# Kernel tuning notes

Hardware: AMD Instinct MI355X
Metric: run time of the kernel (lower is better)

## Reference

```python
import jax, jax.numpy as jnp
import numpy as np

N_NODES = 40000
N_EDGES = 320000
IN_DIM = 256
HID = 128
HEADS = 4
N_GAT = 3  # num_layers - 1
EPS = 1e-5
NEG_SLOPE = 0.2  # PyG GATConv default


def setup_inputs() -> dict:
    key = jax.random.key(0)
    ks = jax.random.split(key, 16)
    s = 0.05
    return {
        "x": jax.random.normal(ks[0], (N_NODES, IN_DIM), jnp.float32),
        "edge_index": jax.random.randint(ks[1], (2, N_EDGES), 0, N_NODES, jnp.int64),
        "proj_W": jax.random.normal(ks[2], (IN_DIM, HID), jnp.float32) * s,
        "proj_b": jnp.zeros((HID,), jnp.float32),
        "gat_W": jax.random.normal(ks[3], (N_GAT, HID, HEADS * HID), jnp.float32) * s,
        "gat_att_src": jax.random.normal(ks[4], (N_GAT, HEADS, HID), jnp.float32) * s,
        "gat_att_dst": jax.random.normal(ks[5], (N_GAT, HEADS, HID), jnp.float32) * s,
        "gat_bias": jnp.zeros((N_GAT, HID), jnp.float32),
        "ln_gamma": jnp.ones((N_GAT, HID), jnp.float32),
        "ln_beta": jnp.zeros((N_GAT, HID), jnp.float32),
        "gcn_W": jax.random.normal(ks[6], (HID, 1), jnp.float32) * s,
        "gcn_b": jnp.zeros((1,), jnp.float32),
    }


def reference(x, edge_index, proj_W, proj_b, gat_W, gat_att_src, gat_att_dst,
              gat_bias, ln_gamma, ln_beta, gcn_W, gcn_b):
    N = x.shape[0]
    loops = jnp.arange(N)
    src = jnp.concatenate([edge_index[0], loops])  # add_self_loops=True
    dst = jnp.concatenate([edge_index[1], loops])

    h = x @ proj_W + proj_b  # [N, HID]

    for i in range(N_GAT):
        identity = h
        xh = (h @ gat_W[i]).reshape(N, HEADS, HID)      # [N, H, C]
        a_s = jnp.einsum("nhc,hc->nh", xh, gat_att_src[i])  # [N, H]
        a_d = jnp.einsum("nhc,hc->nh", xh, gat_att_dst[i])
        e = jax.nn.leaky_relu(a_s[src] + a_d[dst], NEG_SLOPE)  # [E, H]
        # segment softmax over incoming edges per dst node
        m = jax.ops.segment_max(e, dst, num_segments=N)
        ex = jnp.exp(e - m[dst])
        denom = jax.ops.segment_sum(ex, dst, num_segments=N)
        alpha = ex / denom[dst]                         # [E, H]
        agg = jax.ops.segment_sum(xh[src] * alpha[:, :, None], dst, num_segments=N)
        h = agg.mean(axis=1) + gat_bias[i]              # concat=False -> head mean
        # LayerNorm (biased variance, eps=1e-5)
        mu = h.mean(-1, keepdims=True)
        var = ((h - mu) ** 2).mean(-1, keepdims=True)
        h = (h - mu) * jax.lax.rsqrt(var + EPS) * ln_gamma[i] + ln_beta[i]
        h = jax.nn.relu(h)
        # dropout: inference mode -> identity
        h = h + identity

    # GCNConv(hidden, 1) with symmetric normalization and self loops
    deg = jax.ops.segment_sum(jnp.ones_like(dst, dtype=h.dtype), dst, num_segments=N)
    dinv = jax.lax.rsqrt(deg)  # deg >= 1 due to self loops
    norm = dinv[src] * dinv[dst]                        # [E]
    xw = h @ gcn_W                                      # [N, 1]
    out = jax.ops.segment_sum(xw[src] * norm[:, None], dst, num_segments=N) + gcn_b
    return jax.nn.sigmoid(out).reshape(-1)
```

## Files before the change

kernel.cpp:

```cpp
#include <hip/hip_runtime.h>
#include <math.h>

#define INDIM 256
#define HID 128
#define HEADS 4
#define NGAT 3
#define LN_EPS 1e-5f
#define SLOPE 0.2f
#define MPAD 40064
#define LOG2E 1.4426950408889634f

typedef __attribute__((ext_vector_type(8))) short short8;
typedef __attribute__((ext_vector_type(4))) float f32x4;

__device__ inline float wsum(float v) {
#pragma unroll
  for (int m = 1; m < 64; m <<= 1) v += __shfl_xor(v, m, 64);
  return v;
}
__device__ inline float wmax(float v) {
#pragma unroll
  for (int m = 1; m < 64; m <<= 1) v = fmaxf(v, __shfl_xor(v, m, 64));
  return v;
}
__device__ inline float lk2(float v) { return fmaxf(v, SLOPE * v) * LOG2E; }
__device__ inline float sel4(float a0, float a1, float a2, float a3, int i) {
  float lo = (i & 1) ? a1 : a0;
  float hi = (i & 1) ? a3 : a2;
  return (i & 2) ? hi : lo;
}

__device__ inline unsigned short f2b(float f) {
  unsigned u = __float_as_uint(f);
  unsigned r = (u + 0x7FFFu + ((u >> 16) & 1u)) >> 16;
  return (unsigned short)r;
}
__device__ inline float b2f(unsigned short b) {
  return __uint_as_float(((unsigned)b) << 16);
}
__device__ inline void unp8(const uint4 v, float f[8]) {
  f[0] = __uint_as_float(v.x << 16);
  f[1] = __uint_as_float(v.x & 0xFFFF0000u);
  f[2] = __uint_as_float(v.y << 16);
  f[3] = __uint_as_float(v.y & 0xFFFF0000u);
  f[4] = __uint_as_float(v.z << 16);
  f[5] = __uint_as_float(v.z & 0xFFFF0000u);
  f[6] = __uint_as_float(v.w << 16);
  f[7] = __uint_as_float(v.w & 0xFFFF0000u);
}

__device__ __host__ inline size_t fidx(int row, int k, int K) {
  return ((size_t)(row >> 4) * (K >> 5) + (k >> 5)) * 512 +
         ((((k >> 3) & 3) * 16 + (row & 15)) << 3) + (k & 7);
}

__global__ void k_deg(const int* __restrict__ ei, int E, int N, int* __restrict__ deg) {
  int e = blockIdx.x * blockDim.x + threadIdx.x;
  if (e >= E + N) return;
  int dst = (e < E) ? ei[E + e] : (e - E);
  atomicAdd(&deg[dst], 1);
}

__global__ void k_scan1(const int* __restrict__ deg, int N, int* __restrict__ bsums) {
  __shared__ int s[256];
  int gid = blockIdx.x * 256 + threadIdx.x;
  s[threadIdx.x] = (gid < N) ? deg[gid] : 0;
  __syncthreads();
  for (int off = 128; off > 0; off >>= 1) {
    if (threadIdx.x < off) s[threadIdx.x] += s[threadIdx.x + off];
    __syncthreads();
  }
  if (threadIdx.x == 0) bsums[blockIdx.x] = s[0];
}

__global__ void k_scan2(int* __restrict__ bsums, int nblk, int* __restrict__ rowptr, int N) {
  __shared__ int s[256];
  int t = threadIdx.x;
  int v = (t < nblk) ? bsums[t] : 0;
  s[t] = v;
  __syncthreads();
  for (int off = 1; off < 256; off <<= 1) {
    int u = (t >= off) ? s[t - off] : 0;
    __syncthreads();
    s[t] += u;
    __syncthreads();
  }
  if (t < nblk) bsums[t] = s[t] - v;
  if (t == nblk - 1) rowptr[N] = s[t];
}

__global__ void k_scan3(const int* __restrict__ deg, int N, const int* __restrict__ bsums,
                        int* __restrict__ rowptr, int* __restrict__ cursor,
                        float* __restrict__ dinv) {
  __shared__ int s[256];
  int gid = blockIdx.x * 256 + threadIdx.x;
  int v = (gid < N) ? deg[gid] : 0;
  s[threadIdx.x] = v;
  __syncthreads();
  for (int off = 1; off < 256; off <<= 1) {
    int t = (threadIdx.x >= off) ? s[threadIdx.x - off] : 0;
    __syncthreads();
    s[threadIdx.x] += t;
    __syncthreads();
  }
  if (gid < N) {
    int ex = bsums[blockIdx.x] + s[threadIdx.x] - v;
    rowptr[gid] = ex;
    cursor[gid] = ex;
    dinv[gid] = rsqrtf((float)v);
  }
}

__global__ void k_fill(const int* __restrict__ ei, int E, int N,
                       int* __restrict__ cursor, int* __restrict__ csr) {
  int e = blockIdx.x * blockDim.x + threadIdx.x;
  if (e >= E + N) return;
  int src, dst;
  if (e < E) { src = ei[e]; dst = ei[E + e]; } else { src = dst = e - E; }
  int pos = atomicAdd(&cursor[dst], 1);
  csr[pos] = src;
}

__global__ void k_wprep(const float* __restrict__ Wp, const float* __restrict__ Wg,
                        unsigned short* __restrict__ WtPF,
                        unsigned short* __restrict__ Wt2F) {
  int idx = blockIdx.x * 256 + threadIdx.x;
  if (idx < INDIM * HID) {
    int k = idx >> 7, c = idx & 127;
    WtPF[fidx(c, k, INDIM)] = f2b(Wp[idx]);
    return;
  }
  idx -= INDIM * HID;
  if (idx >= NGAT * HID * HEADS * HID) return;
  int l = idx / (HID * HEADS * HID);
  int rem = idx - l * HID * HEADS * HID;
  int k = rem >> 9;
  int cc = rem & 511;
  int hh = cc >> 7, c = cc & 127;
  Wt2F[(size_t)l * (HID * HEADS * HID) + fidx(c, hh * HID + k, HEADS * HID)] =
      f2b(Wg[idx] * 0.25f);
}

__global__ void k_xfrag(const float* __restrict__ x, unsigned short* __restrict__ xbF,
                        int N) {
  int t = blockIdx.x * 256 + threadIdx.x;
  if (t >= MPAD * 32) return;
  int n = t >> 5, kc = t & 31;
  uint4 pk = make_uint4(0, 0, 0, 0);
  if (n < N) {
    const float* ap = x + (size_t)n * INDIM + kc * 8;
    float4 u = *(const float4*)ap;
    float4 v = *(const float4*)(ap + 4);
    pk.x = (unsigned)f2b(u.x) | ((unsigned)f2b(u.y) << 16);
    pk.y = (unsigned)f2b(u.z) | ((unsigned)f2b(u.w) << 16);
    pk.z = (unsigned)f2b(v.x) | ((unsigned)f2b(v.y) << 16);
    pk.w = (unsigned)f2b(v.z) | ((unsigned)f2b(v.w) << 16);
  }
  size_t addr = ((size_t)(n >> 4) * 8 + (kc >> 2)) * 512 +
                (((kc & 3) * 16 + (n & 15)) << 3);
  *(uint4*)(xbF + addr) = pk;
}

__global__ void k_wvec(const float* __restrict__ W, const float* __restrict__ atts,
                       const float* __restrict__ attd, float* __restrict__ w_s,
                       float* __restrict__ w_d) {
  int lane = threadIdx.x & 63;
  int idx = blockIdx.x * 4 + (threadIdx.x >> 6);
  if (idx >= NGAT * HEADS * HID) return;
  int l = idx / (HEADS * HID);
  int rem = idx - l * (HEADS * HID);
  int hh = rem >> 7, k = rem & 127;
  const float2 w2 = *(const float2*)(W + ((size_t)(l * HID + k)) * (HEADS * HID) +
                                     hh * HID + lane * 2);
  const float2 s2 = *(const float2*)(atts + (size_t)(l * HEADS + hh) * HID + lane * 2);
  const float2 d2 = *(const float2*)(attd + (size_t)(l * HEADS + hh) * HID + lane * 2);
  float ps = w2.x * s2.x + w2.y * s2.y;
  float pd = w2.x * d2.x + w2.y * d2.y;
  ps = wsum(ps);
  pd = wsum(pd);
  if (lane == 0) { w_s[idx] = ps; w_d[idx] = pd; }
}

__global__ __launch_bounds__(256) void k_mm(
    const unsigned short* __restrict__ xbF, const unsigned short* __restrict__ WtPF,
    const float* __restrict__ bias, const float* __restrict__ ws0,
    const float* __restrict__ wd0, unsigned short* __restrict__ hb,
    float* __restrict__ a_s, float* __restrict__ a_d) {
  const int wid = threadIdx.x >> 6;
  const int lane = threadIdx.x & 63;
  const int l15 = lane & 15;
  const int g = lane >> 4;
  const int row0 = blockIdx.x * 64 + wid * 16;
  f32x4 acc[8] = {};
  const unsigned short* Ap = xbF + (size_t)(row0 >> 4) * 8 * 512 + lane * 8;
  const unsigned short* Bp = WtPF + lane * 8;
  for (int kb = 0; kb < 8; ++kb) {
    short8 af = *(const short8*)(Ap + kb * 512);
    short8 bfr[8];
#pragma unroll
    for (int ni = 0; ni < 8; ++ni)
      bfr[ni] = *(const short8*)(Bp + (size_t)(ni * 8 + kb) * 512);
#pragma unroll
    for (int ni = 0; ni < 8; ++ni)
      acc[ni] = __builtin_amdgcn_mfma_f32_16x16x32_bf16(af, bfr[ni], acc[ni], 0, 0, 0);
  }
#pragma unroll
  for (int r = 0; r < 4; ++r) {
    const int row = row0 + g * 4 + r;
    unsigned short* hbr = hb + (size_t)row * HID;
    float yv[8];
#pragma unroll
    for (int ni = 0; ni < 8; ++ni) {
      const int c = ni * 16 + l15;
      yv[ni] = acc[ni][r] + bias[c];
      hbr[c] = f2b(yv[ni]);
    }
    float ps[4], pd[4];
#pragma unroll
    for (int h4 = 0; h4 < 4; ++h4) {
      float pv = 0.f, qv = 0.f;
#pragma unroll
      for (int ni = 0; ni < 8; ++ni) {
        const int c = h4 * HID + ni * 16 + l15;
        pv = fmaf(yv[ni], ws0[c], pv);
        qv = fmaf(yv[ni], wd0[c], qv);
      }
#pragma unroll
      for (int m = 1; m < 16; m <<= 1) {
        pv += __shfl_xor(pv, m, 64);
        qv += __shfl_xor(qv, m, 64);
      }
      ps[h4] = pv;
      pd[h4] = qv;
    }
    if (l15 == 0) {
      *(float4*)(a_s + (size_t)row * 4) = make_float4(ps[0], ps[1], ps[2], ps[3]);
      *(float4*)(a_d + (size_t)row * 4) = make_float4(pd[0], pd[1], pd[2], pd[3]);
    }
  }
}

__global__ __launch_bounds__(256) void k_agg2(
    const int* __restrict__ rowptr, const int* __restrict__ csr,
    const unsigned short* __restrict__ hb, const float* __restrict__ a_s,
    const float* __restrict__ a_d, unsigned short* __restrict__ aggF, int N) {
  __shared__ int s_lds[4][64];
  __shared__ float al_lds[4][4][68];
  int lane = threadIdx.x & 63;
  int wid = threadIdx.x >> 6;
  int n = blockIdx.x * 4 + wid;
  if (n >= MPAD) return;
  const int g = lane >> 4;
  const int l15 = lane & 15;
  size_t oaddr = ((size_t)(n >> 4) * 16 + (g * 4 + (l15 >> 2))) * 512 +
                 (((l15 & 3) * 16 + (n & 15)) << 3);
  if (n >= N) {
    *(uint4*)(aggF + oaddr) = make_uint4(0, 0, 0, 0);
    return;
  }
  int beg = rowptr[n], end = rowptr[n + 1];
  int deg = end - beg;
  const unsigned short* hbase = hb + l15 * 8;
  float acc[8] = {};
  float f[8];
  if (deg <= 64) {
    const float ad = a_d[n * 4 + g];
    int sj[4];
    float ex[4];
    float mymax = -3e38f;
#pragma unroll
    for (int j = 0; j < 4; ++j) {
      int e = beg + l15 + 16 * j;
      bool v = e < end;
      int s = v ? csr[e] : 0;
      sj[j] = s;
      float Lv = v ? lk2(a_s[s * 4 + g] + ad) : -3e38f;
      ex[j] = Lv;
      mymax = fmaxf(mymax, Lv);
    }
#pragma unroll
    for (int m = 1; m < 16; m <<= 1) mymax = fmaxf(mymax, __shfl_xor(mymax, m, 64));
    float mysum = 0.f;
#pragma unroll
    for (int j = 0; j < 4; ++j) {
      ex[j] = exp2f(ex[j] - mymax);
      mysum += ex[j];
    }
#pragma unroll
    for (int m = 1; m < 16; m <<= 1) mysum += __shfl_xor(mysum, m, 64);
    float r = 1.f / mysum;
#pragma unroll
    for (int j = 0; j < 4; ++j) {
      int i = l15 + 16 * j;
      al_lds[wid][g][i] = ex[j] * r;
      if (g == 0) s_lds[wid][i] = sj[j];
    }
    asm volatile("s_waitcnt lgkmcnt(0)" ::: "memory");
    const int* sw = s_lds[wid];
    const float* aw = al_lds[wid][g];
    int nIter = (deg + 3) >> 2;
    for (int it = 0; it < nIter; ++it) {
      int4 s4 = *(const int4*)(sw + it * 4);
      float4 a4 = *(const float4*)(aw + it * 4);
      uint4 r0 = *(const uint4*)(hbase + (size_t)s4.x * HID);
      uint4 r1 = *(const uint4*)(hbase + (size_t)s4.y * HID);
      uint4 r2 = *(const uint4*)(hbase + (size_t)s4.z * HID);
      uint4 r3 = *(const uint4*)(hbase + (size_t)s4.w * HID);
      unp8(r0, f);
#pragma unroll
      for (int j = 0; j < 8; ++j) acc[j] = fmaf(a4.x, f[j], acc[j]);
      unp8(r1, f);
#pragma unroll
      for (int j = 0; j < 8; ++j) acc[j] = fmaf(a4.y, f[j], acc[j]);
      unp8(r2, f);
#pragma unroll
      for (int j = 0; j < 8; ++j) acc[j] = fmaf(a4.z, f[j], acc[j]);
      unp8(r3, f);
#pragma unroll
      for (int j = 0; j < 8; ++j) acc[j] = fmaf(a4.w, f[j], acc[j]);
    }
  } else {
    const float4 adv = *(const float4*)(a_d + (size_t)n * 4);
    float m0 = -3e38f, m1 = -3e38f, m2 = -3e38f, m3 = -3e38f;
    for (int e = beg + lane; e < end; e += 64) {
      int s = csr[e];
      const float4 asv = *(const float4*)(a_s + (size_t)s * 4);
      m0 = fmaxf(m0, lk2(asv.x + adv.x));
      m1 = fmaxf(m1, lk2(asv.y + adv.y));
      m2 = fmaxf(m2, lk2(asv.z + adv.z));
      m3 = fmaxf(m3, lk2(asv.w + adv.w));
    }
    m0 = wmax(m0); m1 = wmax(m1); m2 = wmax(m2); m3 = wmax(m3);
    float d0 = 0.f, d1 = 0.f, d2 = 0.f, d3 = 0.f;
    for (int e = beg + lane; e < end; e += 64) {
      int s = csr[e];
      const float4 asv = *(const float4*)(a_s + (size_t)s * 4);
      d0 += exp2f(lk2(asv.x + adv.x) - m0);
      d1 += exp2f(lk2(asv.y + adv.y) - m1);
      d2 += exp2f(lk2(asv.z + adv.z) - m2);
      d3 += exp2f(lk2(asv.w + adv.w) - m3);
    }
    float r0 = 1.f / wsum(d0);
    float r1 = 1.f / wsum(d1);
    float r2 = 1.f / wsum(d2);
    float r3 = 1.f / wsum(d3);
    for (int sb = beg; sb < end; sb += 64) {
      int e = sb + lane;
      bool val = e < end;
      int s = csr[val ? e : end - 1];
      const float4 asv = *(const float4*)(a_s + (size_t)s * 4);
      float q0 = val ? exp2f(lk2(asv.x + adv.x) - m0) * r0 : 0.f;
      float q1 = val ? exp2f(lk2(asv.y + adv.y) - m1) * r1 : 0.f;
      float q2 = val ? exp2f(lk2(asv.z + adv.z) - m2) * r2 : 0.f;
      float q3 = val ? exp2f(lk2(asv.w + adv.w) - m3) * r3 : 0.f;
      int cnt = min(64, end - sb);
      for (int i = 0; i < cnt; ++i) {
        int si = __shfl(s, i, 64);
        float c0 = __shfl(q0, i, 64), c1 = __shfl(q1, i, 64);
        float c2 = __shfl(q2, i, 64), c3 = __shfl(q3, i, 64);
        uint4 hv = *(const uint4*)(hbase + (size_t)si * HID);
        float bi = sel4(c0, c1, c2, c3, g);
        unp8(hv, f);
#pragma unroll
        for (int j = 0; j < 8; ++j) acc[j] = fmaf(bi, f[j], acc[j]);
      }
    }
  }
  uint4 pk;
  pk.x = (unsigned)f2b(acc[0]) | ((unsigned)f2b(acc[1]) << 16);
  pk.y = (unsigned)f2b(acc[2]) | ((unsigned)f2b(acc[3]) << 16);
  pk.z = (unsigned)f2b(acc[4]) | ((unsigned)f2b(acc[5]) << 16);
  pk.w = (unsigned)f2b(acc[6]) | ((unsigned)f2b(acc[7]) << 16);
  *(uint4*)(aggF + oaddr) = pk;
}

template <int ATT>
__global__ __launch_bounds__(256) void k_mm2(
    const unsigned short* __restrict__ aggF, const unsigned short* __restrict__ Bt,
    const float* __restrict__ bias, const float* __restrict__ gamma,
    const float* __restrict__ beta, const float* __restrict__ wsn,
    const float* __restrict__ wdn, unsigned short* __restrict__ hb,
    float* __restrict__ a_s, float* __restrict__ a_d, float* __restrict__ xw) {
  const int wid = threadIdx.x >> 6;
  const int lane = threadIdx.x & 63;
  const int l15 = lane & 15;
  const int g = lane >> 4;
  const int row0 = blockIdx.x * 64 + wid * 16;
  f32x4 acc[8] = {};
  const unsigned short* Ap = aggF + (size_t)(row0 >> 4) * 16 * 512 + lane * 8;
  const unsigned short* Bp = Bt + lane * 8;
  for (int kb = 0; kb < 16; ++kb) {
    short8 a0 = *(const short8*)(Ap + kb * 512);
    short8 bfr[8];
#pragma unroll
    for (int ni = 0; ni < 8; ++ni)
      bfr[ni] = *(const short8*)(Bp + (size_t)(ni * 16 + kb) * 512);
#pragma unroll
    for (int ni = 0; ni < 8; ++ni)
      acc[ni] = __builtin_amdgcn_mfma_f32_16x16x32_bf16(a0, bfr[ni], acc[ni], 0, 0, 0);
  }
  float gm[8], bt8[8];
#pragma unroll
  for (int ni = 0; ni < 8; ++ni) {
    int c = ni * 16 + l15;
    gm[ni] = gamma[c];
    bt8[ni] = beta[c];
    float bs = bias[c];
#pragma unroll
    for (int r = 0; r < 4; ++r) acc[ni][r] += bs;
  }
#pragma unroll
  for (int r = 0; r < 4; ++r) {
    float s = 0.f;
#pragma unroll
    for (int ni = 0; ni < 8; ++ni) s += acc[ni][r];
#pragma unroll
    for (int m = 1; m < 16; m <<= 1) s += __shfl_xor(s, m, 64);
    float mu = s * (1.f / 128.f);
    float q = 0.f;
#pragma unroll
    for (int ni = 0; ni < 8; ++ni) {
      float dd = acc[ni][r] - mu;
      q += dd * dd;
    }
#pragma unroll
    for (int m = 1; m < 16; m <<= 1) q += __shfl_xor(q, m, 64);
    float rstd = rsqrtf(q * (1.f / 128.f) + LN_EPS);
    const int row = row0 + g * 4 + r;
    unsigned short* hbr = hb + (size_t)row * HID;
    float yv[8];
#pragma unroll
    for (int ni = 0; ni < 8; ++ni) {
      int c = ni * 16 + l15;
      float y = (acc[ni][r] - mu) * rstd * gm[ni] + bt8[ni];
      y = fmaxf(y, 0.f) + b2f(hbr[c]);
      hbr[c] = f2b(y);
      yv[ni] = y;
    }
    if (ATT == 1) {
      float ps[4], pd[4];
#pragma unroll
      for (int h4 = 0; h4 < 4; ++h4) {
        float pv = 0.f, qv = 0.f;
#pragma unroll
        for (int ni = 0; ni < 8; ++ni) {
          const int c = h4 * HID + ni * 16 + l15;
          pv = fmaf(yv[ni], wsn[c], pv);
          qv = fmaf(yv[ni], wdn[c], qv);
        }
#pragma unroll
        for (int m = 1; m < 16; m <<= 1) {
          pv += __shfl_xor(pv, m, 64);
          qv += __shfl_xor(qv, m, 64);
        }
        ps[h4] = pv;
        pd[h4] = qv;
      }
      if (l15 == 0) {
        *(float4*)(a_s + (size_t)row * 4) = make_float4(ps[0], ps[1], ps[2], ps[3]);
        *(float4*)(a_d + (size_t)row * 4) = make_float4(pd[0], pd[1], pd[2], pd[3]);
      }
    } else {
      float pv = 0.f;
#pragma unroll
      for (int ni = 0; ni < 8; ++ni) pv = fmaf(yv[ni], wsn[ni * 16 + l15], pv);
#pragma unroll
      for (int m = 1; m < 16; m <<= 1) pv += __shfl_xor(pv, m, 64);
      if (l15 == 0) xw[row] = pv;
    }
  }
}

__global__ __launch_bounds__(256) void k_gcn(const int* __restrict__ rowptr,
                                             const int* __restrict__ csr,
                                             const float* __restrict__ xw,
                                             const float* __restrict__ dinv,
                                             const float* __restrict__ gcn_b,
                                             float* __restrict__ out, int N) {
  int n = blockIdx.x * blockDim.x + threadIdx.x;
  if (n >= N) return;
  float acc = 0.f;
  int beg = rowptr[n], end = rowptr[n + 1];
  for (int e = beg; e < end; ++e) {
    int s = csr[e];
    acc += xw[s] * dinv[s];
  }
  float z = acc * dinv[n] + gcn_b[0];
  out[n] = 1.f / (1.f + expf(-z));
}

extern "C" void kernel_launch(void* const* d_in, const int* in_sizes, int n_in,
                              void* d_out, int out_size, void* d_ws, size_t ws_size,
                              hipStream_t stream) {
  const float* x = (const float*)d_in[0];
  const int* ei = (const int*)d_in[1];
  const float* proj_W = (const float*)d_in[2];
  const float* proj_b = (const float*)d_in[3];
  const float* gat_W = (const float*)d_in[4];
  const float* gat_as = (const float*)d_in[5];
  const float* gat_ad = (const float*)d_in[6];
  const float* gat_bias = (const float*)d_in[7];
  const float* ln_g = (const float*)d_in[8];
  const float* ln_b = (const float*)d_in[9];
  const float* gcn_W = (const float*)d_in[10];
  const float* gcn_b = (const float*)d_in[11];
  float* out = (float*)d_out;

  const int N = in_sizes[0] / INDIM;
  const int E = in_sizes[1] / 2;
  const int TOT = E + N;

  size_t off = 0;
  auto alloc = [&](size_t bytes) {
    void* p = (char*)d_ws + off;
    off += (bytes + 255) & ~(size_t)255;
    return p;
  };
  unsigned short* hb = (unsigned short*)alloc((size_t)MPAD * HID * 2);
  unsigned short* aggF = (unsigned short*)alloc((size_t)MPAD * HEADS * HID * 2);
  unsigned short* xbF = (unsigned short*)alloc((size_t)MPAD * INDIM * 2);
  unsigned short* WtPF = (unsigned short*)alloc((size_t)HID * INDIM * 2);
  unsigned short* Wt2F = (unsigned short*)alloc((size_t)NGAT * HID * HEADS * HID * 2);
  float* w_s = (float*)alloc((size_t)NGAT * HEADS * HID * 4);
  float* w_d = (float*)alloc((size_t)NGAT * HEADS * HID * 4);
  float* a_s = (float*)alloc((size_t)MPAD * HEADS * 4);
  float* a_d = (float*)alloc((size_t)MPAD * HEADS * 4);
  int* deg = (int*)alloc((size_t)N * 4);
  int* rowptr = (int*)alloc((size_t)(N + 1) * 4);
  int* cursor = (int*)alloc((size_t)N * 4);
  int* csr = (int*)alloc((size_t)TOT * 4);
  int* bsums = (int*)alloc(1024);
  float* dinv = (float*)alloc((size_t)N * 4);
  float* xw = (float*)alloc((size_t)MPAD * 4);
  (void)ws_size;

  const int NBLK = (N + 255) / 256;
  const int EBLK = (TOT + 255) / 256;

  hipMemsetAsync(deg, 0, (size_t)N * 4, stream);
  k_deg<<<EBLK, 256, 0, stream>>>(ei, E, N, deg);
  k_scan1<<<NBLK, 256, 0, stream>>>(deg, N, bsums);
  k_scan2<<<1, 256, 0, stream>>>(bsums, NBLK, rowptr, N);
  k_scan3<<<NBLK, 256, 0, stream>>>(deg, N, bsums, rowptr, cursor, dinv);
  k_fill<<<EBLK, 256, 0, stream>>>(ei, E, N, cursor, csr);

  const int WPN = INDIM * HID + NGAT * HID * HEADS * HID;
  k_wprep<<<(WPN + 255) / 256, 256, 0, stream>>>(proj_W, gat_W, WtPF, Wt2F);
  k_wvec<<<(NGAT * HEADS * HID + 3) / 4, 256, 0, stream>>>(gat_W, gat_as, gat_ad, w_s, w_d);
  k_xfrag<<<(MPAD * 32 + 255) / 256, 256, 0, stream>>>(x, xbF, N);

  k_mm<<<MPAD / 64, 256, 0, stream>>>(xbF, WtPF, proj_b, w_s, w_d, hb, a_s, a_d);

  for (int i = 0; i < NGAT; ++i) {
    k_agg2<<<MPAD / 4, 256, 0, stream>>>(rowptr, csr, hb, a_s, a_d, aggF, N);
    if (i < NGAT - 1) {
      k_mm2<1><<<MPAD / 64, 256, 0, stream>>>(
          aggF, Wt2F + (size_t)i * HID * HEADS * HID, gat_bias + (size_t)i * HID,
          ln_g + (size_t)i * HID, ln_b + (size_t)i * HID,
          w_s + (size_t)(i + 1) * HEADS * HID, w_d + (size_t)(i + 1) * HEADS * HID,
          hb, a_s, a_d, nullptr);
    } else {
      k_mm2<2><<<MPAD / 64, 256, 0, stream>>>(
          aggF, Wt2F + (size_t)i * HID * HEADS * HID, gat_bias + (size_t)i * HID,
          ln_g + (size_t)i * HID, ln_b + (size_t)i * HID, gcn_W, nullptr,
          hb, nullptr, nullptr, xw);
    }
  }

  k_gcn<<<NBLK, 256, 0, stream>>>(rowptr, csr, xw, dinv, gcn_b, out, N);
}
```

Before: 280.3 us.

## Fuse x bf16 conversion into projection GEMM and prescale GCN features

```diff
diff --git a/kernel.cpp b/kernel.cpp
--- a/kernel.cpp
+++ b/kernel.cpp
@@ -139,26 +139,6 @@
   int hh = cc >> 7, c = cc & 127;
   Wt2F[(size_t)l * (HID * HEADS * HID) + fidx(c, hh * HID + k, HEADS * HID)] =
       f2b(Wg[idx] * 0.25f);
-}
-
-__global__ void k_xfrag(const float* __restrict__ x, unsigned short* __restrict__ xbF,
-                        int N) {
-  int t = blockIdx.x * 256 + threadIdx.x;
-  if (t >= MPAD * 32) return;
-  int n = t >> 5, kc = t & 31;
-  uint4 pk = make_uint4(0, 0, 0, 0);
-  if (n < N) {
-    const float* ap = x + (size_t)n * INDIM + kc * 8;
-    float4 u = *(const float4*)ap;
-    float4 v = *(const float4*)(ap + 4);
-    pk.x = (unsigned)f2b(u.x) | ((unsigned)f2b(u.y) << 16);
-    pk.y = (unsigned)f2b(u.z) | ((unsigned)f2b(u.w) << 16);
-    pk.z = (unsigned)f2b(v.x) | ((unsigned)f2b(v.y) << 16);
-    pk.w = (unsigned)f2b(v.z) | ((unsigned)f2b(v.w) << 16);
-  }
-  size_t addr = ((size_t)(n >> 4) * 8 + (kc >> 2)) * 512 +
-                (((kc & 3) * 16 + (n & 15)) << 3);
-  *(uint4*)(xbF + addr) = pk;
 }
 
 __global__ void k_wvec(const float* __restrict__ W, const float* __restrict__ atts,
@@ -182,20 +162,38 @@
 }
 
 __global__ __launch_bounds__(256) void k_mm(
-    const unsigned short* __restrict__ xbF, const unsigned short* __restrict__ WtPF,
+    const float* __restrict__ x, const unsigned short* __restrict__ WtPF,
     const float* __restrict__ bias, const float* __restrict__ ws0,
     const float* __restrict__ wd0, unsigned short* __restrict__ hb,
-    float* __restrict__ a_s, float* __restrict__ a_d) {
+    float* __restrict__ a_s, float* __restrict__ a_d, int Mreal) {
+  __shared__ unsigned short As[64 * INDIM];
   const int wid = threadIdx.x >> 6;
   const int lane = threadIdx.x & 63;
   const int l15 = lane & 15;
   const int g = lane >> 4;
   const int row0 = blockIdx.x * 64 + wid * 16;
+#pragma unroll
+  for (int i = 0; i < 8; ++i) {
+    int p = threadIdx.x + 256 * i;
+    int nl = p >> 5, kc = p & 31;
+    int grow = blockIdx.x * 64 + nl;
+    uint4 pk = make_uint4(0, 0, 0, 0);
+    if (grow < Mreal) {
+      const float* ap = x + (size_t)grow * INDIM + kc * 8;
+      float4 u = *(const float4*)ap;
+      float4 v = *(const float4*)(ap + 4);
+      pk.x = (unsigned)f2b(u.x) | ((unsigned)f2b(u.y) << 16);
+      pk.y = (unsigned)f2b(u.z) | ((unsigned)f2b(u.w) << 16);
+      pk.z = (unsigned)f2b(v.x) | ((unsigned)f2b(v.y) << 16);
+      pk.w = (unsigned)f2b(v.z) | ((unsigned)f2b(v.w) << 16);
+    }
+    *(uint4*)&As[((nl >> 4) * 8 + (kc >> 2)) * 512 + (((kc & 3) * 16 + (nl & 15)) << 3)] = pk;
+  }
+  __syncthreads();
   f32x4 acc[8] = {};
-  const unsigned short* Ap = xbF + (size_t)(row0 >> 4) * 8 * 512 + lane * 8;
   const unsigned short* Bp = WtPF + lane * 8;
   for (int kb = 0; kb < 8; ++kb) {
-    short8 af = *(const short8*)(Ap + kb * 512);
+    short8 af = *(const short8*)&As[(wid * 8 + kb) * 512 + lane * 8];
     short8 bfr[8];
 #pragma unroll
     for (int ni = 0; ni < 8; ++ni)
@@ -380,7 +378,8 @@
     const float* __restrict__ bias, const float* __restrict__ gamma,
     const float* __restrict__ beta, const float* __restrict__ wsn,
     const float* __restrict__ wdn, unsigned short* __restrict__ hb,
-    float* __restrict__ a_s, float* __restrict__ a_d, float* __restrict__ xw) {
+    float* __restrict__ a_s, float* __restrict__ a_d,
+    const float* __restrict__ dinvp, float* __restrict__ xwd) {
   const int wid = threadIdx.x >> 6;
   const int lane = threadIdx.x & 63;
   const int l15 = lane & 15;
@@ -466,14 +465,14 @@
       for (int ni = 0; ni < 8; ++ni) pv = fmaf(yv[ni], wsn[ni * 16 + l15], pv);
 #pragma unroll
       for (int m = 1; m < 16; m <<= 1) pv += __shfl_xor(pv, m, 64);
-      if (l15 == 0) xw[row] = pv;
+      if (l15 == 0) xwd[row] = pv * dinvp[row];
     }
   }
 }
 
 __global__ __launch_bounds__(256) void k_gcn(const int* __restrict__ rowptr,
                                              const int* __restrict__ csr,
-                                             const float* __restrict__ xw,
+                                             const float* __restrict__ xwd,
                                              const float* __restrict__ dinv,
                                              const float* __restrict__ gcn_b,
                                              float* __restrict__ out, int N) {
@@ -481,10 +480,13 @@
   if (n >= N) return;
   float acc = 0.f;
   int beg = rowptr[n], end = rowptr[n + 1];
-  for (int e = beg; e < end; ++e) {
-    int s = csr[e];
-    acc += xw[s] * dinv[s];
-  }
+  int e = beg;
+  for (; e + 4 <= end; e += 4) {
+    int s0 = csr[e], s1 = csr[e + 1], s2 = csr[e + 2], s3 = csr[e + 3];
+    float v0 = xwd[s0], v1 = xwd[s1], v2 = xwd[s2], v3 = xwd[s3];
+    acc += (v0 + v1) + (v2 + v3);
+  }
+  for (; e < end; ++e) acc += xwd[csr[e]];
   float z = acc * dinv[n] + gcn_b[0];
   out[n] = 1.f / (1.f + expf(-z));
 }
@@ -518,7 +520,6 @@
   };
   unsigned short* hb = (unsigned short*)alloc((size_t)MPAD * HID * 2);
   unsigned short* aggF = (unsigned short*)alloc((size_t)MPAD * HEADS * HID * 2);
-  unsigned short* xbF = (unsigned short*)alloc((size_t)MPAD * INDIM * 2);
   unsigned short* WtPF = (unsigned short*)alloc((size_t)HID * INDIM * 2);
   unsigned short* Wt2F = (unsigned short*)alloc((size_t)NGAT * HID * HEADS * HID * 2);
   float* w_s = (float*)alloc((size_t)NGAT * HEADS * HID * 4);
@@ -530,8 +531,8 @@
   int* cursor = (int*)alloc((size_t)N * 4);
   int* csr = (int*)alloc((size_t)TOT * 4);
   int* bsums = (int*)alloc(1024);
-  float* dinv = (float*)alloc((size_t)N * 4);
-  float* xw = (float*)alloc((size_t)MPAD * 4);
+  float* dinv = (float*)alloc((size_t)MPAD * 4);
+  float* xwd = (float*)alloc((size_t)MPAD * 4);
   (void)ws_size;
 
   const int NBLK = (N + 255) / 256;
@@ -547,9 +548,8 @@
   const int WPN = INDIM * HID + NGAT * HID * HEADS * HID;
   k_wprep<<<(WPN + 255) / 256, 256, 0, stream>>>(proj_W, gat_W, WtPF, Wt2F);
   k_wvec<<<(NGAT * HEADS * HID + 3) / 4, 256, 0, stream>>>(gat_W, gat_as, gat_ad, w_s, w_d);
-  k_xfrag<<<(MPAD * 32 + 255) / 256, 256, 0, stream>>>(x, xbF, N);
-
-  k_mm<<<MPAD / 64, 256, 0, stream>>>(xbF, WtPF, proj_b, w_s, w_d, hb, a_s, a_d);
+
+  k_mm<<<MPAD / 64, 256, 0, stream>>>(x, WtPF, proj_b, w_s, w_d, hb, a_s, a_d, N);
 
   for (int i = 0; i < NGAT; ++i) {
     k_agg2<<<MPAD / 4, 256, 0, stream>>>(rowptr, csr, hb, a_s, a_d, aggF, N);
@@ -558,14 +558,14 @@
           aggF, Wt2F + (size_t)i * HID * HEADS * HID, gat_bias + (size_t)i * HID,
           ln_g + (size_t)i * HID, ln_b + (size_t)i * HID,
           w_s + (size_t)(i + 1) * HEADS * HID, w_d + (size_t)(i + 1) * HEADS * HID,
-          hb, a_s, a_d, nullptr);
+          hb, a_s, a_d, nullptr, nullptr);
     } else {
       k_mm2<2><<<MPAD / 64, 256, 0, stream>>>(
           aggF, Wt2F + (size_t)i * HID * HEADS * HID, gat_bias + (size_t)i * HID,
           ln_g + (size_t)i * HID, ln_b + (size_t)i * HID, gcn_W, nullptr,
-          hb, nullptr, nullptr, xw);
-    }
-  }
-
-  k_gcn<<<NBLK, 256, 0, stream>>>(rowptr, csr, xw, dinv, gcn_b, out, N);
-}
+          hb, nullptr, nullptr, dinv, xwd);
+    }
+  }
+
+  k_gcn<<<NBLK, 256, 0, stream>>>(rowptr, csr, xwd, dinv, gcn_b, out, N);
+}
```

Result: faster. 271.3 us (-3.2%).
